# Kernel tuning notes

Measured on AMD Instinct MI355X. Metric: run time of the kernel, lower is better.

## Reference

```python
import jax, jax.numpy as jnp
import numpy as np

N = 100_000      # nodes
E = 1_000_000    # edges
F_IN = 32        # num_features
F_OUT = 32       # out_channels
K = 3            # num_filters (diffusion steps)


def setup_inputs() -> dict:
    key = jax.random.key(0)
    ks = jax.random.split(key, 12)
    d_in = F_IN + F_OUT  # gates see concat([X, H])
    s = 1.0 / np.sqrt(d_in)
    inp = {
        "x": jax.random.normal(ks[0], (N, F_IN), jnp.float32),
        "edge_index": jax.random.randint(ks[1], (2, E), 0, N, dtype=jnp.int32),
        "edge_weight": jax.random.uniform(ks[2], (E,), jnp.float32, 0.01, 1.0),
        "h": jnp.zeros((N, F_OUT), jnp.float32),
        "c": jnp.zeros((N, F_OUT), jnp.float32),
        # DConv weights: [2 directions, K hops, d_in, F_OUT] per gate
        "Wz": s * jax.random.normal(ks[3], (2, K, d_in, F_OUT), jnp.float32),
        "bz": jnp.zeros((F_OUT,), jnp.float32),
        "Wr": s * jax.random.normal(ks[4], (2, K, d_in, F_OUT), jnp.float32),
        "br": jnp.zeros((F_OUT,), jnp.float32),
        "Wh": s * jax.random.normal(ks[5], (2, K, d_in, F_OUT), jnp.float32),
        "bh": jnp.zeros((F_OUT,), jnp.float32),
        "Wl": s * jax.random.normal(ks[6], (F_OUT, 1), jnp.float32),
        "bl": jnp.zeros((1,), jnp.float32),
    }
    return inp


def _dconv(X, src, dst, ew, W, b):
    """Bidirectional K-hop diffusion conv (DCRNN DConv). X: [N, d_in]."""
    n = X.shape[0]
    deg_out = jax.ops.segment_sum(ew, src, num_segments=n)  # weighted out-degree
    deg_in = jax.ops.segment_sum(ew, dst, num_segments=n)   # weighted in-degree
    norm_out = ew / deg_out[src]  # D_out^{-1} W random walk
    norm_in = ew / deg_in[dst]    # D_in^{-1} W^T random walk

    def prop_out(v):  # forward diffusion: aggregate at dst from src
        return jax.ops.segment_sum(norm_out[:, None] * v[src], dst, num_segments=n)

    def prop_in(v):   # reverse diffusion: aggregate at src from dst
        return jax.ops.segment_sum(norm_in[:, None] * v[dst], src, num_segments=n)

    H = X @ W[0, 0] + X @ W[1, 0]
    Kk = W.shape[1]
    if Kk > 1:
        T0o = T0i = X
        T1o, T1i = prop_out(X), prop_in(X)
        H = H + T1o @ W[0, 1] + T1i @ W[1, 1]
        for k in range(2, Kk):
            T2o = 2.0 * prop_out(T1o) - T0o
            T2i = 2.0 * prop_in(T1i) - T0i
            H = H + T2o @ W[0, k] + T2i @ W[1, k]
            T0o, T1o = T1o, T2o
            T0i, T1i = T1i, T2i
    return H + b


def reference(x, edge_index, edge_weight, h, c, Wz, bz, Wr, br, Wh, bh, Wl, bl):
    src, dst = edge_index[0], edge_index[1]
    # wrapper passes H=None (h_1 = None) -> hidden state initialized to zeros
    H0 = jnp.zeros((x.shape[0], F_OUT), x.dtype)
    XH = jnp.concatenate([x, H0], axis=1)
    Z = jax.nn.sigmoid(_dconv(XH, src, dst, edge_weight, Wz, bz))
    R = jax.nn.sigmoid(_dconv(XH, src, dst, edge_weight, Wr, br))
    XRH = jnp.concatenate([x, R * H0], axis=1)
    H_tilde = jnp.tanh(_dconv(XRH, src, dst, edge_weight, Wh, bh))
    H = Z * H0 + (1.0 - Z) * H_tilde  # GRU update
    y = jax.nn.relu(H) @ Wl + bl      # relu + linear head
    return y
```

## Files before the change

kernel.cpp:

```cpp
#include <hip/hip_runtime.h>
#include <math.h>

#define NN 100000
#define NE 1000000
#define F 32
#define NBKT 196
#define BKT2 (2 * NBKT)
#define CAPB 5888
#define CAPP 8192
#define EB 4096
#define NTILE 6250
#define BUCKB 245
#define CONV512 782
#define MEGAB (BUCKB + CONV512 + 20)

typedef unsigned short ushortT;
typedef unsigned int uintT;
typedef __attribute__((ext_vector_type(8))) short short8;
typedef __attribute__((ext_vector_type(4))) float f32x4;

__device__ inline float bfhi(uintT u)  { return __int_as_float(u & 0xffff0000u); }
__device__ inline float bflo(uintT u)  { return __int_as_float(u << 16); }
__device__ inline uintT f2bf(float f) {
    uintT u = __float_as_uint(f);
    return (u + 0x7fffu + ((u >> 16) & 1u)) >> 16;
}
__device__ inline uintT pack15(float f) {
    uintT u = __float_as_uint(f);
    return ((u + 0x7fffu + ((u >> 16) & 1u)) >> 16) & 0x7fffu;
}
__device__ inline float unpack15(uintT v) { return __int_as_float((v & 0x7fffu) << 16); }

__launch_bounds__(512)
__global__ void k_mega(const int* __restrict__ ei, const float* __restrict__ ew,
                       int* __restrict__ cursor, uint2* __restrict__ stg,
                       const float* __restrict__ x, ushortT* __restrict__ xbr,
                       const float* __restrict__ Wz, const float* __restrict__ Wh,
                       ushortT* __restrict__ wfrag) {
    const int tid = threadIdx.x;

    if (blockIdx.x >= BUCKB) {
        int rb = blockIdx.x - BUCKB;
        if (rb < CONV512) {
            int i = rb * 512 + tid;
            if (i >= NN * F / 8) return;
            const float4* p = (const float4*)x + (long)i * 2;
            float4 a = p[0], b = p[1];
            uint4 o;
            o.x = f2bf(a.x) | (f2bf(a.y) << 16);
            o.y = f2bf(a.z) | (f2bf(a.w) << 16);
            o.z = f2bf(b.x) | (f2bf(b.y) << 16);
            o.w = f2bf(b.z) | (f2bf(b.w) << 16);
            ((uint4*)xbr)[i] = o;
            return;
        }
        int gid = (rb - CONV512) * 512 + tid;
        int f = gid >> 9, rem = gid & 511;
        int l = rem >> 3, r = rem & 7;
        int kc = f >> 2, nt = f & 3;
        int n = nt * 16 + (l & 15);
        int fi = (l >> 4) * 8 + r;
        int jc = n & 31;
        const float* W = (n >= 32) ? Wh : Wz;
#define WDK(d, k) W[((((d) * 3 + (k)) * 64) + fi) * 32 + jc]
        float v;
        if      (kc == 0) v = WDK(0,0) + WDK(1,0) - WDK(0,2) - WDK(1,2);
        else if (kc == 1) v = WDK(0,1);
        else if (kc == 2) v = WDK(1,1);
        else if (kc == 3) v = 2.0f * WDK(0,2);
        else              v = 2.0f * WDK(1,2);
#undef WDK
        wfrag[gid] = (ushortT)f2bf(v);
        return;
    }

    __shared__ int cntL[BKT2], baseL[BKT2];

    const int e0 = blockIdx.x * EB;

    for (int b = tid; b < BKT2; b += 512) cntL[b] = 0;
    __syncthreads();

    int     rs[EB / 512];
    int     rd[EB / 512];
    uintT   rw[EB / 512];
    ushortT rr0[EB / 512];
    ushortT rr1[EB / 512];
#pragma unroll
    for (int k = 0; k < EB / 512; ++k) {
        int gid = e0 + tid + k * 512;
        int s = -1, d = -1; uintT w = 0; int r0 = 0, r1 = 0;
        if (gid < NE) {
            s = ei[gid]; d = ei[NE + gid]; w = pack15(ew[gid]);
            r0 = atomicAdd(&cntL[d >> 9], 1);
            r1 = atomicAdd(&cntL[NBKT + (s >> 9)], 1);
        }
        rs[k] = s; rd[k] = d; rw[k] = w;
        rr0[k] = (ushortT)r0; rr1[k] = (ushortT)r1;
    }
    __syncthreads();

    for (int b = tid; b < BKT2; b += 512) {
        int c = cntL[b];
        if (c > 0) baseL[b] = atomicAdd(&cursor[b], c);
    }
    __syncthreads();

#pragma unroll
    for (int k = 0; k < EB / 512; ++k) {
        int s = rs[k];
        if (s < 0) continue;
        int d = rd[k]; uintT w = rw[k];
        int b0 = d >> 9;
        int p0 = baseL[b0] + rr0[k];
        if (p0 < CAPB) stg[(size_t)b0 * CAPB + p0] = make_uint2(((uintT)s << 15) | w, (uintT)(d & 511));
        int b1 = NBKT + (s >> 9);
        int p1 = baseL[b1] + rr1[k];
        if (p1 < CAPB) stg[(size_t)b1 * CAPB + p1] = make_uint2(((uintT)d << 15) | w, (uintT)(s & 511));
    }
}

__launch_bounds__(512)
__global__ void k_csr(const int* __restrict__ cursor, const uint2* __restrict__ stg,
                      uintT* __restrict__ entF, int2* __restrict__ meta,
                      float* __restrict__ rdeg) {
    __shared__ int   ncnt[512];
    __shared__ int   nbase[512];
    __shared__ float wsum[512];
    __shared__ int   wavesum[8];
    __shared__ int   totS;
    __shared__ uintT entV[CAPP];

    const int b   = blockIdx.x;
    const int tid = threadIdx.x;
    const int dir = (b >= NBKT) ? 1 : 0;
    const int n0  = (dir ? (b - NBKT) : b) << 9;
    const int c   = min(cursor[b], CAPB);
    const uint2* S = stg + (size_t)b * CAPB;

    ncnt[tid] = 0; wsum[tid] = 0.f;
#pragma unroll
    for (int k = 0; k < CAPP / 512; ++k) entV[tid + k * 512] = 0u;
    __syncthreads();

    uint2   sv[12];
    ushortT rk[12];
#pragma unroll
    for (int k = 0; k < 12; ++k) {
        int i = tid + k * 512;
        if (i < c) {
            uint2 it = S[i];
            sv[k] = it;
            rk[k] = (ushortT)atomicAdd(&ncnt[it.y], 1);
            atomicAdd(&wsum[it.y], unpack15(it.x));
        }
    }
    __syncthreads();

    int sp = ncnt[tid];
    int pc = (sp + 7) & ~7;
    int lane = tid & 63, wid = tid >> 6;
    int incl = pc;
#pragma unroll
    for (int o = 1; o < 64; o <<= 1) {
        int t = __shfl_up(incl, o, 64);
        if (lane >= o) incl += t;
    }
    if (lane == 63) wavesum[wid] = incl;
    __syncthreads();
    int woff = 0;
    for (int wq = 0; wq < wid; ++wq) woff += wavesum[wq];
    nbase[tid] = incl - pc + woff;
    if (tid == 511) totS = min(incl + woff, CAPP);
    __syncthreads();

    const int rb = b * CAPP;
    {
        int node = n0 + tid;
        if (node < NN) {
            int seg = dir * NN + node;
            meta[seg] = make_int2(rb + nbase[tid], pc);
            float s = wsum[tid];
            rdeg[seg] = 1.0f / ((s > 0.f) ? s : 1.0f);
        }
    }

#pragma unroll
    for (int k = 0; k < 12; ++k) {
        int i = tid + k * 512;
        if (i < c) {
            uint2 it = sv[k];
            int pos = nbase[it.y] + rk[k];
            if (pos < CAPP) entV[pos] = it.x;
        }
    }
    __syncthreads();

    const int t4 = totS >> 2;
    for (int i = tid; i < t4; i += 512) {
        uint4 v = make_uint4(entV[4 * i], entV[4 * i + 1], entV[4 * i + 2], entV[4 * i + 3]);
        *(uint4*)(entF + rb + 4 * i) = v;
    }
}

__launch_bounds__(256)
__global__ void k_hop(const int2* __restrict__ meta, const uintT* __restrict__ entF,
                      const float* __restrict__ rdeg,
                      const ushortT* __restrict__ fo, const ushortT* __restrict__ fi,
                      ushortT* __restrict__ oo, ushortT* __restrict__ oi) {
    const int dir = blockIdx.x & 1;
    const int n   = (blockIdx.x >> 1) * 32 + (threadIdx.x >> 3);
    if (n >= NN) return;
    const int q   = threadIdx.x & 7;
    const int2 m  = meta[dir * NN + n];
    const int opp = dir ? 0 : NN;
    const ushortT* __restrict__ feat = dir ? fi : fo;

    float ax = 0.f, ay = 0.f, az = 0.f, aw = 0.f;
    const int end = m.x + m.y;
    for (int p = m.x; p < end; p += 8) {
        float nms[8]; uint2 vs[8];
#pragma unroll
        for (int k = 0; k < 8; ++k) {
            uintT en = entF[p + k];
            int idx = (int)(en >> 15);
            nms[k] = unpack15(en) * rdeg[opp + idx];
            vs[k]  = *(const uint2*)(feat + (long)idx * F + q * 4);
        }
#pragma unroll
        for (int k = 0; k < 8; ++k) {
            ax += nms[k] * bflo(vs[k].x);
            ay += nms[k] * bfhi(vs[k].x);
            az += nms[k] * bflo(vs[k].y);
            aw += nms[k] * bfhi(vs[k].y);
        }
    }
    uint2 o = make_uint2(f2bf(ax) | (f2bf(ay) << 16), f2bf(az) | (f2bf(aw) << 16));
    *(uint2*)((dir ? oi : oo) + (long)n * F + q * 4) = o;
}

__launch_bounds__(256)
__global__ void k_final(const ushortT* __restrict__ xb,
                        const ushortT* __restrict__ t1o, const ushortT* __restrict__ t1i,
                        const ushortT* __restrict__ p2o, const ushortT* __restrict__ p2i,
                        const ushortT* __restrict__ wfrag,
                        const float* __restrict__ bz, const float* __restrict__ bh,
                        const float* __restrict__ Wl, const float* __restrict__ bl,
                        float* __restrict__ y, int nwaves) {
    const int lane = threadIdx.x & 63;
    const int wgid = blockIdx.x * 4 + (threadIdx.x >> 6);
    const int quad = lane >> 4;
    const int c0   = lane & 15;

    union U8 { uint4 u; short8 s; };

    short8 bfr[20];
#pragma unroll
    for (int f = 0; f < 20; ++f) {
        U8 t; t.u = *(const uint4*)(wfrag + f * 512 + lane * 8);
        bfr[f] = t.s;
    }

    const float bz0 = bz[c0], bz1 = bz[c0 + 16];
    const float bh0 = bh[c0], bh1 = bh[c0 + 16];
    const float wl0 = Wl[c0], wl1 = Wl[c0 + 16];
    const float blv = bl[0];

    const ushortT* srcs[5] = {xb, t1o, t1i, p2o, p2i};

    for (int t = wgid; t < NTILE; t += nwaves) {
        const long off = (long)t * 16 * F + (long)c0 * F + quad * 8;
        f32x4 a0 = {0.f, 0.f, 0.f, 0.f}, a1 = a0, a2 = a0, a3 = a0;
#pragma unroll
        for (int kc = 0; kc < 5; ++kc) {
            U8 av; av.u = *(const uint4*)(srcs[kc] + off);
            a0 = __builtin_amdgcn_mfma_f32_16x16x32_bf16(av.s, bfr[kc * 4 + 0], a0, 0, 0, 0);
            a1 = __builtin_amdgcn_mfma_f32_16x16x32_bf16(av.s, bfr[kc * 4 + 1], a1, 0, 0, 0);
            a2 = __builtin_amdgcn_mfma_f32_16x16x32_bf16(av.s, bfr[kc * 4 + 2], a2, 0, 0, 0);
            a3 = __builtin_amdgcn_mfma_f32_16x16x32_bf16(av.s, bfr[kc * 4 + 3], a3, 0, 0, 0);
        }
        float res[4];
#pragma unroll
        for (int r = 0; r < 4; ++r) {
            float gz = a0[r] + bz0, gh = a2[r] + bh0;
            float z  = 1.0f / (1.0f + __expf(-gz));
            float e2 = __expf(2.0f * gh);
            float ht = 1.0f - 2.0f / (e2 + 1.0f);
            float v  = fmaxf((1.0f - z) * ht, 0.0f) * wl0;
            gz = a1[r] + bz1; gh = a3[r] + bh1;
            z  = 1.0f / (1.0f + __expf(-gz));
            e2 = __expf(2.0f * gh);
            ht = 1.0f - 2.0f / (e2 + 1.0f);
            v += fmaxf((1.0f - z) * ht, 0.0f) * wl1;
            res[r] = v;
        }
#pragma unroll
        for (int o = 1; o < 16; o <<= 1) {
            res[0] += __shfl_xor(res[0], o, 64);
            res[1] += __shfl_xor(res[1], o, 64);
            res[2] += __shfl_xor(res[2], o, 64);
            res[3] += __shfl_xor(res[3], o, 64);
        }
        if (c0 == 0) {
            f32x4 out = {res[0] + blv, res[1] + blv, res[2] + blv, res[3] + blv};
            *(f32x4*)(y + t * 16 + quad * 4) = out;
        }
    }
}

extern "C" void kernel_launch(void* const* d_in, const int* in_sizes, int n_in,
                              void* d_out, int out_size, void* d_ws, size_t ws_size,
                              hipStream_t stream) {
    const float* x  = (const float*)d_in[0];
    const int*   ei = (const int*)  d_in[1];
    const float* ew = (const float*)d_in[2];
    const float* Wz = (const float*)d_in[5];
    const float* bz = (const float*)d_in[6];
    const float* Wh = (const float*)d_in[9];
    const float* bh = (const float*)d_in[10];
    const float* Wl = (const float*)d_in[11];
    const float* bl = (const float*)d_in[12];
    float* y = (float*)d_out;

    const long NFW = (long)NN * F;
    int*     cursor = (int*)d_ws;
    int2*    meta   = (int2*)(cursor + 512);
    float*   rdeg   = (float*)(meta + 2 * NN);
    uintT*   entF   = (uintT*)(rdeg + 2 * NN);
    ushortT* wfrag  = (ushortT*)(entF + (size_t)BKT2 * CAPP);
    ushortT* xbr    = wfrag + 10240;
    ushortT* t1o    = xbr + NFW;
    ushortT* t1i    = t1o + NFW;
    ushortT* p2o    = t1i + NFW;
    ushortT* p2i    = p2o + NFW;
    uint2*   stg    = (uint2*)(p2i + NFW);

    hipMemsetAsync(cursor, 0, 512 * sizeof(int), stream);

    k_mega<<<MEGAB, 512, 0, stream>>>(ei, ew, cursor, stg, x, xbr, Wz, Wh, wfrag);
    k_csr<<<BKT2, 512, 0, stream>>>(cursor, stg, entF, meta, rdeg);
    k_hop<<<2 * ((NN + 31) / 32), 256, 0, stream>>>(meta, entF, rdeg, xbr, xbr, t1o, t1i);
    k_hop<<<2 * ((NN + 31) / 32), 256, 0, stream>>>(meta, entF, rdeg, t1o, t1i, p2o, p2i);
    const int fblocks = 521;
    k_final<<<fblocks, 256, 0, stream>>>(xbr, t1o, t1i, p2o, p2i, wfrag,
                                         bz, bh, Wl, bl, y, fblocks * 4);
}
```

Measured before the change: 210.6 us.

## Fuse second diffusion hop into final MFMA gate kernel via shared memory

Merges the second k_hop launch and k_final into one kernel. Each 256-thread block gathers the second-hop aggregates for its 64 nodes into LDS and then runs the MFMA gate, GRU and linear head on them directly. This drops the p2o/p2i global write and read-back and one kernel launch. The cost is that the final stage loses its persistent grid-stride loop and the gather's load imbalance now stalls the MFMA work at the block barrier.

Result: no change. 213.2 us (+1.2%).

```diff
diff --git a/kernel.cpp b/kernel.cpp
--- a/kernel.cpp
+++ b/kernel.cpp
@@ -13,6 +13,7 @@
 #define BUCKB 245
 #define CONV512 782
 #define MEGAB (BUCKB + CONV512 + 20)
+#define HFINB 1563
 
 typedef unsigned short ushortT;
 typedef unsigned int uintT;
@@ -240,25 +241,67 @@
 }
 
 __launch_bounds__(256)
-__global__ void k_final(const ushortT* __restrict__ xb,
-                        const ushortT* __restrict__ t1o, const ushortT* __restrict__ t1i,
-                        const ushortT* __restrict__ p2o, const ushortT* __restrict__ p2i,
-                        const ushortT* __restrict__ wfrag,
-                        const float* __restrict__ bz, const float* __restrict__ bh,
-                        const float* __restrict__ Wl, const float* __restrict__ bl,
-                        float* __restrict__ y, int nwaves) {
-    const int lane = threadIdx.x & 63;
-    const int wgid = blockIdx.x * 4 + (threadIdx.x >> 6);
+__global__ void k_hfin(const int2* __restrict__ meta, const uintT* __restrict__ entF,
+                       const float* __restrict__ rdeg,
+                       const ushortT* __restrict__ xb,
+                       const ushortT* __restrict__ t1o, const ushortT* __restrict__ t1i,
+                       const ushortT* __restrict__ wfrag,
+                       const float* __restrict__ bz, const float* __restrict__ bh,
+                       const float* __restrict__ Wl, const float* __restrict__ bl,
+                       float* __restrict__ y) {
+    __shared__ uint2 p2l[2][64][8];
+
+    const int tid = threadIdx.x;
+    const int n0  = blockIdx.x * 64;
+
+    const int g = tid >> 3, q = tid & 7;
+#pragma unroll
+    for (int pass = 0; pass < 4; ++pass) {
+        const int dir = pass >> 1;
+        const int l   = ((pass & 1) << 5) + g;
+        const int n   = n0 + l;
+        float ax = 0.f, ay = 0.f, az = 0.f, aw = 0.f;
+        if (n < NN) {
+            const int2 m  = meta[dir * NN + n];
+            const int opp = dir ? 0 : NN;
+            const ushortT* __restrict__ feat = dir ? t1i : t1o;
+            const int end = m.x + m.y;
+            for (int p = m.x; p < end; p += 8) {
+                float nms[8]; uint2 vs[8];
+#pragma unroll
+                for (int k = 0; k < 8; ++k) {
+                    uintT en = entF[p + k];
+                    int idx = (int)(en >> 15);
+                    nms[k] = unpack15(en) * rdeg[opp + idx];
+                    vs[k]  = *(const uint2*)(feat + (long)idx * F + q * 4);
+                }
+#pragma unroll
+                for (int k = 0; k < 8; ++k) {
+                    ax += nms[k] * bflo(vs[k].x);
+                    ay += nms[k] * bfhi(vs[k].x);
+                    az += nms[k] * bflo(vs[k].y);
+                    aw += nms[k] * bfhi(vs[k].y);
+                }
+            }
+        }
+        p2l[dir][l][q] = make_uint2(f2bf(ax) | (f2bf(ay) << 16),
+                                    f2bf(az) | (f2bf(aw) << 16));
+    }
+    __syncthreads();
+
+    const int wv = tid >> 6;
+    const int t  = blockIdx.x * 4 + wv;
+    if (t >= NTILE) return;
+    const int lane = tid & 63;
     const int quad = lane >> 4;
     const int c0   = lane & 15;
 
     union U8 { uint4 u; short8 s; };
-
     short8 bfr[20];
 #pragma unroll
     for (int f = 0; f < 20; ++f) {
-        U8 t; t.u = *(const uint4*)(wfrag + f * 512 + lane * 8);
-        bfr[f] = t.s;
+        U8 tt; tt.u = *(const uint4*)(wfrag + f * 512 + lane * 8);
+        bfr[f] = tt.s;
     }
 
     const float bz0 = bz[c0], bz1 = bz[c0 + 16];
@@ -266,45 +309,51 @@
     const float wl0 = Wl[c0], wl1 = Wl[c0 + 16];
     const float blv = bl[0];
 
-    const ushortT* srcs[5] = {xb, t1o, t1i, p2o, p2i};
-
-    for (int t = wgid; t < NTILE; t += nwaves) {
-        const long off = (long)t * 16 * F + (long)c0 * F + quad * 8;
-        f32x4 a0 = {0.f, 0.f, 0.f, 0.f}, a1 = a0, a2 = a0, a3 = a0;
-#pragma unroll
-        for (int kc = 0; kc < 5; ++kc) {
-            U8 av; av.u = *(const uint4*)(srcs[kc] + off);
-            a0 = __builtin_amdgcn_mfma_f32_16x16x32_bf16(av.s, bfr[kc * 4 + 0], a0, 0, 0, 0);
-            a1 = __builtin_amdgcn_mfma_f32_16x16x32_bf16(av.s, bfr[kc * 4 + 1], a1, 0, 0, 0);
-            a2 = __builtin_amdgcn_mfma_f32_16x16x32_bf16(av.s, bfr[kc * 4 + 2], a2, 0, 0, 0);
-            a3 = __builtin_amdgcn_mfma_f32_16x16x32_bf16(av.s, bfr[kc * 4 + 3], a3, 0, 0, 0);
-        }
-        float res[4];
-#pragma unroll
-        for (int r = 0; r < 4; ++r) {
-            float gz = a0[r] + bz0, gh = a2[r] + bh0;
-            float z  = 1.0f / (1.0f + __expf(-gz));
-            float e2 = __expf(2.0f * gh);
-            float ht = 1.0f - 2.0f / (e2 + 1.0f);
-            float v  = fmaxf((1.0f - z) * ht, 0.0f) * wl0;
-            gz = a1[r] + bz1; gh = a3[r] + bh1;
-            z  = 1.0f / (1.0f + __expf(-gz));
-            e2 = __expf(2.0f * gh);
-            ht = 1.0f - 2.0f / (e2 + 1.0f);
-            v += fmaxf((1.0f - z) * ht, 0.0f) * wl1;
-            res[r] = v;
-        }
-#pragma unroll
-        for (int o = 1; o < 16; o <<= 1) {
-            res[0] += __shfl_xor(res[0], o, 64);
-            res[1] += __shfl_xor(res[1], o, 64);
-            res[2] += __shfl_xor(res[2], o, 64);
-            res[3] += __shfl_xor(res[3], o, 64);
-        }
-        if (c0 == 0) {
-            f32x4 out = {res[0] + blv, res[1] + blv, res[2] + blv, res[3] + blv};
-            *(f32x4*)(y + t * 16 + quad * 4) = out;
-        }
+    const long off = (long)t * 16 * F + (long)c0 * F + quad * 8;
+    f32x4 a0 = {0.f, 0.f, 0.f, 0.f}, a1 = a0, a2 = a0, a3 = a0;
+    const ushortT* gsrcs[3] = {xb, t1o, t1i};
+#pragma unroll
+    for (int kc = 0; kc < 3; ++kc) {
+        U8 av; av.u = *(const uint4*)(gsrcs[kc] + off);
+        a0 = __builtin_amdgcn_mfma_f32_16x16x32_bf16(av.s, bfr[kc * 4 + 0], a0, 0, 0, 0);
+        a1 = __builtin_amdgcn_mfma_f32_16x16x32_bf16(av.s, bfr[kc * 4 + 1], a1, 0, 0, 0);
+        a2 = __builtin_amdgcn_mfma_f32_16x16x32_bf16(av.s, bfr[kc * 4 + 2], a2, 0, 0, 0);
+        a3 = __builtin_amdgcn_mfma_f32_16x16x32_bf16(av.s, bfr[kc * 4 + 3], a3, 0, 0, 0);
+    }
+#pragma unroll
+    for (int kc = 3; kc < 5; ++kc) {
+        U8 av; av.u = *(const uint4*)&p2l[kc - 3][wv * 16 + c0][quad * 2];
+        a0 = __builtin_amdgcn_mfma_f32_16x16x32_bf16(av.s, bfr[kc * 4 + 0], a0, 0, 0, 0);
+        a1 = __builtin_amdgcn_mfma_f32_16x16x32_bf16(av.s, bfr[kc * 4 + 1], a1, 0, 0, 0);
+        a2 = __builtin_amdgcn_mfma_f32_16x16x32_bf16(av.s, bfr[kc * 4 + 2], a2, 0, 0, 0);
+        a3 = __builtin_amdgcn_mfma_f32_16x16x32_bf16(av.s, bfr[kc * 4 + 3], a3, 0, 0, 0);
+    }
+
+    float res[4];
+#pragma unroll
+    for (int r = 0; r < 4; ++r) {
+        float gz = a0[r] + bz0, gh = a2[r] + bh0;
+        float z  = 1.0f / (1.0f + __expf(-gz));
+        float e2 = __expf(2.0f * gh);
+        float ht = 1.0f - 2.0f / (e2 + 1.0f);
+        float v  = fmaxf((1.0f - z) * ht, 0.0f) * wl0;
+        gz = a1[r] + bz1; gh = a3[r] + bh1;
+        z  = 1.0f / (1.0f + __expf(-gz));
+        e2 = __expf(2.0f * gh);
+        ht = 1.0f - 2.0f / (e2 + 1.0f);
+        v += fmaxf((1.0f - z) * ht, 0.0f) * wl1;
+        res[r] = v;
+    }
+#pragma unroll
+    for (int o = 1; o < 16; o <<= 1) {
+        res[0] += __shfl_xor(res[0], o, 64);
+        res[1] += __shfl_xor(res[1], o, 64);
+        res[2] += __shfl_xor(res[2], o, 64);
+        res[3] += __shfl_xor(res[3], o, 64);
+    }
+    if (c0 == 0) {
+        f32x4 out = {res[0] + blv, res[1] + blv, res[2] + blv, res[3] + blv};
+        *(f32x4*)(y + t * 16 + quad * 4) = out;
     }
 }
 
@@ -331,17 +380,13 @@
     ushortT* xbr    = wfrag + 10240;
     ushortT* t1o    = xbr + NFW;
     ushortT* t1i    = t1o + NFW;
-    ushortT* p2o    = t1i + NFW;
-    ushortT* p2i    = p2o + NFW;
-    uint2*   stg    = (uint2*)(p2i + NFW);
+    uint2*   stg    = (uint2*)(t1i + NFW);
 
     hipMemsetAsync(cursor, 0, 512 * sizeof(int), stream);
 
     k_mega<<<MEGAB, 512, 0, stream>>>(ei, ew, cursor, stg, x, xbr, Wz, Wh, wfrag);
     k_csr<<<BKT2, 512, 0, stream>>>(cursor, stg, entF, meta, rdeg);
     k_hop<<<2 * ((NN + 31) / 32), 256, 0, stream>>>(meta, entF, rdeg, xbr, xbr, t1o, t1i);
-    k_hop<<<2 * ((NN + 31) / 32), 256, 0, stream>>>(meta, entF, rdeg, t1o, t1i, p2o, p2i);
-    const int fblocks = 521;
-    k_final<<<fblocks, 256, 0, stream>>>(xbr, t1o, t1i, p2o, p2i, wfrag,
-                                         bz, bh, Wl, bl, y, fblocks * 4);
-}
+    k_hfin<<<HFINB, 256, 0, stream>>>(meta, entF, rdeg, xbr, t1o, t1i, wfrag,
+                                      bz, bh, Wl, bl, y);
+}
```
